# Kernel optimization log

Measured on AMD Instinct MI355X. Metric: run time of the kernel, lower is better.

## Reference

```python
import jax, jax.numpy as jnp
from jax import lax
import numpy as np

DIM = 8          # per-head dim
BN_EPS = 1e-5
ATT_EPS = 1e-15


def setup_inputs() -> dict:
    key = jax.random.key(0)
    ks = jax.random.split(key, 6)
    B, C, H, W = 2, 512, 128, 128
    total_dim = 512                      # heads(64) * dim(8)
    c3 = 3 * total_dim                   # 1536
    x = jax.random.normal(ks[0], (B, C, H, W), dtype=jnp.float32)
    w_qkv = jax.random.normal(ks[1], (c3, C), dtype=jnp.float32) * 0.02
    w_dw = jax.random.normal(ks[2], (c3, 1, 5, 5), dtype=jnp.float32) * 0.05
    w_pw = jax.random.normal(ks[3], (c3, 8, 1, 1), dtype=jnp.float32) * 0.1
    w_proj = jax.random.normal(ks[4], (512, 2 * total_dim), dtype=jnp.float32) * 0.02
    bn_gamma = jnp.ones((512,), jnp.float32)
    bn_beta = jnp.zeros((512,), jnp.float32)
    bn_mean = jnp.zeros((512,), jnp.float32)
    bn_var = jnp.ones((512,), jnp.float32)
    return {"x": x, "w_qkv": w_qkv, "w_dw": w_dw, "w_pw": w_pw, "w_proj": w_proj,
            "bn_gamma": bn_gamma, "bn_beta": bn_beta, "bn_mean": bn_mean, "bn_var": bn_var}


def reference(x, w_qkv, w_dw, w_pw, w_proj, bn_gamma, bn_beta, bn_mean, bn_var):
    B, C, H, W = x.shape
    dn = ('NCHW', 'OIHW', 'NCHW')
    # qkv: 1x1 conv, no bias/norm/act
    qkv = jnp.einsum('bchw,oc->bohw', x, w_qkv)  # (B, 1536, H, W)
    # multi-scale aggregation: 5x5 depthwise + 1x1 grouped (groups = 3*heads = 192)
    y = lax.conv_general_dilated(qkv, w_dw, (1, 1), [(2, 2), (2, 2)],
                                 feature_group_count=w_dw.shape[0], dimension_numbers=dn)
    y = lax.conv_general_dilated(y, w_pw, (1, 1), [(0, 0), (0, 0)],
                                 feature_group_count=w_pw.shape[0] // w_pw.shape[1],
                                 dimension_numbers=dn)
    mqkv = jnp.concatenate([qkv, y], axis=1)  # (B, 3072, H, W)
    N = H * W
    mqkv = mqkv.reshape(B, -1, 3 * DIM, N)    # (B, 128 heads, 24, N)
    q = jax.nn.relu(mqkv[:, :, :DIM])          # (B, h, d, N)
    k = jax.nn.relu(mqkv[:, :, DIM:2 * DIM])   # (B, h, d, N)
    v = mqkv[:, :, 2 * DIM:]                   # (B, h, d, N)
    v = jnp.pad(v, ((0, 0), (0, 0), (0, 1), (0, 0)), constant_values=1.0)  # (B,h,d+1,N)
    vk = jnp.einsum('bhdn,bhen->bhde', v, k)   # v @ k^T : (B,h,d+1,d)
    out = jnp.einsum('bhde,bhen->bhdn', vk, q)  # (B,h,d+1,N)
    out = out[:, :, :-1] / (out[:, :, -1:] + ATT_EPS)  # (B,h,d,N)
    out = out.reshape(B, -1, H, W)             # (B, 1024, H, W)
    # proj: 1x1 conv + bn2d (inference-mode affine), no act
    out = jnp.einsum('bchw,oc->bohw', out, w_proj)
    inv = bn_gamma / jnp.sqrt(bn_var + BN_EPS)
    out = out * inv[None, :, None, None] + (bn_beta - bn_mean * inv)[None, :, None, None]
    return out
```

## Files before the change

### kernel.cpp

```cpp
#include <hip/hip_runtime.h>

typedef __bf16 bf16_t;
typedef __bf16 bf16x8 __attribute__((ext_vector_type(8)));
typedef __bf16 bf16x4 __attribute__((ext_vector_type(4)));
typedef float  f32x4  __attribute__((ext_vector_type(4)));
typedef _Float16 h16;
typedef _Float16 h16x2 __attribute__((ext_vector_type(2)));
typedef _Float16 h16x4 __attribute__((ext_vector_type(4)));
typedef _Float16 h16x8 __attribute__((ext_vector_type(8)));

#define DEVINL __device__ __forceinline__

static constexpr size_t N_PIX = 16384;

static constexpr size_t OFF_QB  = 0;
static constexpr size_t SZ_QB   = (size_t)512 * N_PIX * 2;
static constexpr size_t OFF_QR  = OFF_QB + SZ_QB;
static constexpr size_t SZ_QR   = SZ_QB;
static constexpr size_t OFF_KV  = OFF_QR + SZ_QR;
static constexpr size_t SZ_KV   = (size_t)1024 * N_PIX * 2;
static constexpr size_t OFF_Y   = OFF_KV + SZ_KV;
static constexpr size_t SZ_Y    = (size_t)1536 * N_PIX * 2;
static constexpr size_t OFF_ATT = OFF_Y + SZ_Y;
static constexpr size_t SZ_ATT  = (size_t)N_PIX * 1024 * 2;
static constexpr size_t OFF_XTH = OFF_ATT;
static constexpr size_t OFF_XTL = OFF_ATT + (size_t)N_PIX * 512 * 2;
static constexpr size_t OFF_WQA = OFF_ATT + SZ_ATT;
static constexpr size_t SZ_WQA  = (size_t)512 * 1536 * 2;
static constexpr size_t OFF_WKV = OFF_WQA + SZ_WQA;
static constexpr size_t SZ_WKV  = (size_t)1024 * 512 * 2;
static constexpr size_t OFF_WP  = OFF_WKV + SZ_WKV;
static constexpr size_t SZ_WP   = (size_t)512 * 1024 * 2;
static constexpr size_t OFF_VK  = OFF_WP + SZ_WP;
static constexpr size_t SZ_VK   = (size_t)128 * 72 * 4;
static constexpr size_t OFF_VKP = OFF_VK + SZ_VK;
static constexpr size_t SZ_VKP  = (size_t)128 * 8 * 72 * 4;
static constexpr size_t OFF_BNA = OFF_VKP + SZ_VKP;
static constexpr size_t OFF_ZP  = OFF_BNA + 2048;
static constexpr size_t OFF_W2  = OFF_ZP + 64;
static constexpr size_t SZ_W2   = (size_t)512 * 1024 * 2;
static constexpr size_t WS_NEEDED = OFF_W2 + SZ_W2;

DEVINL void gload16(const void* g, void* l) {
  __builtin_amdgcn_global_load_lds((const __attribute__((address_space(1))) void*)g,
                                   (__attribute__((address_space(3))) void*)l, 16, 0, 0);
}

__global__ __launch_bounds__(256)
void xpose_kernel(const float* __restrict__ x, bf16_t* __restrict__ xTh, bf16_t* __restrict__ xTl) {
  __shared__ float t[32][33];
  const int n0 = blockIdx.x * 32, c0 = blockIdx.y * 32;
  const int tx = threadIdx.x & 31, ty = threadIdx.x >> 5;
#pragma unroll
  for (int r = 0; r < 4; ++r)
    t[ty + r * 8][tx] = x[(size_t)(c0 + ty + r * 8) * N_PIX + n0 + tx];
  __syncthreads();
  const int nl = threadIdx.x >> 3, sub = threadIdx.x & 7;
  const int c8 = (sub & 3) * 8, plane = sub >> 2;
  bf16x8 o;
#pragma unroll
  for (int k = 0; k < 8; ++k) {
    const float v = t[c8 + k][nl];
    if (plane == 0) {
      o[k] = (bf16_t)v;
    } else {
      const bf16_t hi = (bf16_t)v;
      o[k] = (bf16_t)(v - (float)hi);
    }
  }
  bf16_t* dst = plane ? xTl : xTh;
  *(bf16x8*)&dst[(size_t)(n0 + nl) * 512 + c0 + c8] = o;
}

static constexpr int PREP_W1 = 512 * 1536;
static constexpr int PREP_W2 = 1024 * 512;
static constexpr int PREP_W3 = 512 * 1024;
static constexpr int PREP_TOT = PREP_W1 + PREP_W2 + PREP_W3 + 512 + 16;
__global__ __launch_bounds__(256)
void prep_kernel(const float* __restrict__ wq, const float* __restrict__ wp,
                 const float* __restrict__ gam, const float* __restrict__ bet,
                 const float* __restrict__ mu, const float* __restrict__ va,
                 bf16_t* __restrict__ wqA, bf16_t* __restrict__ wkv, bf16_t* __restrict__ wpb,
                 float* __restrict__ bna, float* __restrict__ zp) {
  const int i = blockIdx.x * 256 + threadIdx.x;
  if (i < PREP_W1) {
    const int r = i / 1536, c = i - r * 1536;
    const int o = (r >> 3) * 24 + (r & 7);
    bf16_t out;
    if (c < 512) {
      out = (bf16_t)wq[o * 512 + c];
    } else if (c < 1024) {
      const float v = wq[o * 512 + c - 512];
      const bf16_t hi = (bf16_t)v;
      out = (bf16_t)(v - (float)hi);
    } else {
      out = (bf16_t)wq[o * 512 + c - 1024];
    }
    wqA[i] = out;
  } else if (i < PREP_W1 + PREP_W2) {
    const int j = i - PREP_W1;
    const int r = j >> 9, c = j & 511;
    const int h = (r & 511) >> 3;
    const int jj = (r < 512 ? 8 : 16) + (r & 7);
    wkv[j] = (bf16_t)wq[(h * 24 + jj) * 512 + c];
  } else if (i < PREP_W1 + PREP_W2 + PREP_W3) {
    const int j = i - PREP_W1 - PREP_W2;
    const int m = j >> 10;
    const float inv = gam[m] / sqrtf(va[m] + 1e-5f);
    wpb[j] = (bf16_t)(wp[j] * inv);
  } else if (i < PREP_W1 + PREP_W2 + PREP_W3 + 512) {
    const int k = i - PREP_W1 - PREP_W2 - PREP_W3;
    const float inv = gam[k] / sqrtf(va[k] + 1e-5f);
    bna[k] = bet[k] - mu[k] * inv;
  } else if (i < PREP_TOT) {
    zp[i - (PREP_W1 + PREP_W2 + PREP_W3 + 512)] = 0.f;
  }
}

__global__ __launch_bounds__(256, 4)
void gemm_qkv_kernel(const bf16_t* __restrict__ wqA, const bf16_t* __restrict__ wkv,
                     const bf16_t* __restrict__ xTh, const bf16_t* __restrict__ xTl,
                     h16* __restrict__ Qb, h16* __restrict__ Qr, h16* __restrict__ KV) {
  __shared__ __align__(16) bf16_t As[128 * 64];
  __shared__ __align__(16) bf16_t Bs[128 * 64];
  const int tid = threadIdx.x, wid = tid >> 6, lane = tid & 63;
  const int fr = lane & 15, fg = lane >> 4;
  const int wm = (wid >> 1) * 64, wn = (wid & 1) * 64;
  const int by = blockIdx.y;
  const bool isQ = by < 4;
  const int m0 = (isQ ? by : by - 4) * 128;
  const int n0 = blockIdx.x * 128;
  const int KA = isQ ? 1536 : 512;
  const bf16_t* Aptr = isQ ? wqA + (size_t)m0 * 1536 : wkv + (size_t)m0 * 512;
  const int srow = tid >> 3;
  const int soff = (((tid & 7) ^ (srow & 7)) * 8);

  f32x4 acc[4][4] = {};

  for (int kk = 0; kk < KA; kk += 64) {
    const bf16_t* Bpl;
    int bcol;
    if (isQ) {
      Bpl  = (kk < 1024) ? xTh : xTl;
      bcol = (kk < 1024) ? (kk & 511) : (kk - 1024);
    } else {
      Bpl = xTh; bcol = kk;
    }
    __syncthreads();
#pragma unroll
    for (int r = 0; r < 4; ++r) {
      gload16(Aptr + (size_t)(srow + 32 * r) * KA + kk + soff, As + (wid * 8 + 32 * r) * 64);
      gload16(Bpl + (size_t)(n0 + srow + 32 * r) * 512 + bcol + soff, Bs + (wid * 8 + 32 * r) * 64);
    }
    __syncthreads();
#pragma unroll
    for (int ks = 0; ks < 2; ++ks) {
      bf16x8 af[4], bfr[4];
#pragma unroll
      for (int i = 0; i < 4; ++i)
        af[i]  = *(const bf16x8*)&As[(wm + i * 16 + fr) * 64 + (((ks * 4 + fg) ^ (fr & 7)) * 8)];
#pragma unroll
      for (int j = 0; j < 4; ++j)
        bfr[j] = *(const bf16x8*)&Bs[(wn + j * 16 + fr) * 64 + (((ks * 4 + fg) ^ (fr & 7)) * 8)];
#pragma unroll
      for (int i = 0; i < 4; ++i)
#pragma unroll
        for (int j = 0; j < 4; ++j)
          acc[i][j] = __builtin_amdgcn_mfma_f32_16x16x32_bf16(af[i], bfr[j], acc[i][j], 0, 0, 0);
    }
  }

#pragma unroll
  for (int i = 0; i < 4; ++i)
#pragma unroll
    for (int r = 0; r < 4; ++r) {
      const int m = m0 + wm + i * 16 + fg * 4 + r;
#pragma unroll
      for (int j = 0; j < 4; ++j) {
        const int n = n0 + wn + j * 16 + fr;
        const float v = acc[i][j][r];
        if (isQ) {
          Qb[(size_t)m * N_PIX + n] = (h16)v;
          Qr[(size_t)m * N_PIX + n] = (h16)fmaxf(0.f, v);
        } else {
          KV[(size_t)m * N_PIX + n] = (h16)v;
        }
      }
    }
}

__global__ __launch_bounds__(256, 4)
void gemm_proj_kernel(const bf16_t* __restrict__ A, const bf16_t* __restrict__ B,
                      float* __restrict__ Cout, const float* __restrict__ bna) {
  __shared__ __align__(16) bf16_t As[128 * 64];
  __shared__ __align__(16) bf16_t Bs[128 * 64];
  const int tid = threadIdx.x, wid = tid >> 6, lane = tid & 63;
  const int fr = lane & 15, fg = lane >> 4;
  const int wm = (wid >> 1) * 64, wn = (wid & 1) * 64;
  const int m0 = blockIdx.y * 128, n0 = blockIdx.x * 128;
  const int srow = tid >> 3;
  const int soff = (((tid & 7) ^ (srow & 7)) * 8);
  const bf16_t* Ab = A + (size_t)m0 * 1024;
  const bf16_t* Bb = B + (size_t)n0 * 1024;

  f32x4 acc[4][4] = {};

  for (int kk = 0; kk < 1024; kk += 64) {
    __syncthreads();
#pragma unroll
    for (int r = 0; r < 4; ++r) {
      gload16(Ab + (size_t)(srow + 32 * r) * 1024 + kk + soff, As + (wid * 8 + 32 * r) * 64);
      gload16(Bb + (size_t)(srow + 32 * r) * 1024 + kk + soff, Bs + (wid * 8 + 32 * r) * 64);
    }
    __syncthreads();
#pragma unroll
    for (int ks = 0; ks < 2; ++ks) {
      bf16x8 af[4], bfr[4];
#pragma unroll
      for (int i = 0; i < 4; ++i)
        af[i]  = *(const bf16x8*)&As[(wm + i * 16 + fr) * 64 + (((ks * 4 + fg) ^ (fr & 7)) * 8)];
#pragma unroll
      for (int j = 0; j < 4; ++j)
        bfr[j] = *(const bf16x8*)&Bs[(wn + j * 16 + fr) * 64 + (((ks * 4 + fg) ^ (fr & 7)) * 8)];
#pragma unroll
      for (int i = 0; i < 4; ++i)
#pragma unroll
        for (int j = 0; j < 4; ++j)
          acc[i][j] = __builtin_amdgcn_mfma_f32_16x16x32_bf16(af[i], bfr[j], acc[i][j], 0, 0, 0);
    }
  }

#pragma unroll
  for (int i = 0; i < 4; ++i)
#pragma unroll
    for (int r = 0; r < 4; ++r) {
      const int m = m0 + wm + i * 16 + fg * 4 + r;
      const float sh = bna[m];
#pragma unroll
      for (int j = 0; j < 4; ++j)
        Cout[(size_t)m * N_PIX + n0 + wn + j * 16 + fr] = acc[i][j][r] + sh;
    }
}

__global__ __launch_bounds__(256)
void dwpw_kernel(const h16* __restrict__ Qb, const h16* __restrict__ KV,
                 const float* __restrict__ wdw, const float* __restrict__ wpw,
                 const h16* __restrict__ zp, h16* __restrict__ y) {
  const int g = blockIdx.y, t = blockIdx.x;
  const int typ = g % 3, head = g / 3;
  const int ty0 = (t >> 1) * 16, tx0 = (t & 1) * 64;
  const int tid = threadIdx.x, wid = tid >> 6, lane = tid & 63;
  __shared__ __align__(16) h16 sin_[8][20][80];
  __shared__ h16x2 swd2[8][25];
  __shared__ h16x2 swp2[8][8];
  if (tid < 200) {
    const h16 w = (h16)wdw[(g * 8 + tid / 25) * 25 + tid % 25];
    h16x2 w2; w2[0] = w; w2[1] = w;
    swd2[tid / 25][tid % 25] = w2;
  }
  if (tid < 64) {
    const h16 w = (h16)wpw[(g * 8 + (tid >> 3)) * 8 + (tid & 7)];
    h16x2 w2; w2[0] = w; w2[1] = w;
    swp2[tid >> 3][tid & 7] = w2;
  }
  const h16* plane = (typ == 0) ? (Qb + (size_t)head * 8 * N_PIX)
                                : (KV + (size_t)((typ == 2 ? 512 : 0) + head * 8) * N_PIX);
  h16* sflat = &sin_[0][0][0];
  for (int base = wid * 64; base < 1600; base += 256) {
    const int id  = base + lane;
    const int ch  = id / 200;
    const int rem = id - ch * 200;
    const int row = rem / 10;
    const int c6  = rem - row * 10;
    const int gy  = ty0 + row - 2;
    const int gx  = tx0 + c6 * 8 - 8;
    const bool ok = ((unsigned)gy < 128u) && ((unsigned)gx < 128u);
    const h16* src = ok ? (plane + (size_t)ch * N_PIX + gy * 128 + gx) : zp;
    gload16(src, sflat + (size_t)base * 8);
  }
  __syncthreads();

  const int px4 = (tid & 15) * 4, py = tid >> 4;
  h16x2 dwa[8][2];
#pragma unroll
  for (int ch = 0; ch < 8; ++ch) {
    h16x2 A0 = 0, A1 = 0;
#pragma unroll
    for (int di = 0; di < 5; ++di) {
      const uint2 w0 = *(const uint2*)&sin_[ch][py + di][px4 + 4];
      const uint2 w1 = *(const uint2*)&sin_[ch][py + di][px4 + 8];
      const uint2 w2v = *(const uint2*)&sin_[ch][py + di][px4 + 12];
      const unsigned u1 = w0.y, u2 = w1.x, u3 = w1.y, u4 = w2v.x;
      const h16x2 P2 = __builtin_bit_cast(h16x2, u1);
      const h16x2 P3 = __builtin_bit_cast(h16x2, (u2 << 16) | (u1 >> 16));
      const h16x2 P4 = __builtin_bit_cast(h16x2, u2);
      const h16x2 P5 = __builtin_bit_cast(h16x2, (u3 << 16) | (u2 >> 16));
      const h16x2 P6 = __builtin_bit_cast(h16x2, u3);
      const h16x2 P7 = __builtin_bit_cast(h16x2, (u4 << 16) | (u3 >> 16));
      const h16x2 P8 = __builtin_bit_cast(h16x2, u4);
      h16x2 wd;
      wd = swd2[ch][di * 5 + 0]; A0 += wd * P2; A1 += wd * P4;
      wd = swd2[ch][di * 5 + 1]; A0 += wd * P3; A1 += wd * P5;
      wd = swd2[ch][di * 5 + 2]; A0 += wd * P4; A1 += wd * P6;
      wd = swd2[ch][di * 5 + 3]; A0 += wd * P5; A1 += wd * P7;
      wd = swd2[ch][di * 5 + 4]; A0 += wd * P6; A1 += wd * P8;
    }
    dwa[ch][0] = A0; dwa[ch][1] = A1;
  }
#pragma unroll
  for (int oc = 0; oc < 8; ++oc) {
    h16x2 o0 = 0, o1 = 0;
#pragma unroll
    for (int ic = 0; ic < 8; ++ic) {
      const h16x2 w = swp2[oc][ic];
      o0 += w * dwa[ic][0];
      o1 += w * dwa[ic][1];
    }
    h16x4 ov; ov[0] = o0[0]; ov[1] = o0[1]; ov[2] = o1[0]; ov[3] = o1[1];
    *(h16x4*)&y[(size_t)(8 * g + oc) * N_PIX + (ty0 + py) * 128 + tx0 + px4] = ov;
  }
}

__global__ __launch_bounds__(256)
void vk_partial_kernel(const h16* __restrict__ KV, const h16* __restrict__ yb,
                       float* __restrict__ part) {
  const int h = blockIdx.y, s = blockIdx.x;
  const h16 *kb, *vb;
  if (h < 64) {
    kb = KV + (size_t)(h * 8) * N_PIX;
    vb = KV + (size_t)(512 + h * 8) * N_PIX;
  } else {
    kb = yb + (size_t)(24 * (h - 64) + 8) * N_PIX;
    vb = yb + (size_t)(24 * (h - 64) + 16) * N_PIX;
  }
  float a[8][8] = {};
  float ak[8] = {};
  const int p0 = s * 2048 + (int)threadIdx.x * 8;
  float kq[8][8], vq[8][8];
#pragma unroll
  for (int e = 0; e < 8; ++e) {
    h16x8 kk = *(const h16x8*)&kb[(size_t)e * N_PIX + p0];
#pragma unroll
    for (int u = 0; u < 8; ++u) kq[e][u] = fmaxf(0.f, (float)kk[u]);
  }
#pragma unroll
  for (int d = 0; d < 8; ++d) {
    h16x8 vv = *(const h16x8*)&vb[(size_t)d * N_PIX + p0];
#pragma unroll
    for (int u = 0; u < 8; ++u) vq[d][u] = (float)vv[u];
  }
#pragma unroll
  for (int d = 0; d < 8; ++d)
#pragma unroll
    for (int e = 0; e < 8; ++e)
#pragma unroll
      for (int u = 0; u < 8; ++u) a[d][e] += vq[d][u] * kq[e][u];
#pragma unroll
  for (int e = 0; e < 8; ++e)
#pragma unroll
    for (int u = 0; u < 8; ++u) ak[e] += kq[e][u];

  __shared__ float red[4][72];
  const int lane = threadIdx.x & 63, wid = threadIdx.x >> 6;
#pragma unroll
  for (int i = 0; i < 72; ++i) {
    float v = (i < 64) ? a[i >> 3][i & 7] : ak[i - 64];
    v += __shfl_xor(v, 32); v += __shfl_xor(v, 16); v += __shfl_xor(v, 8);
    v += __shfl_xor(v, 4);  v += __shfl_xor(v, 2);  v += __shfl_xor(v, 1);
    if (lane == 0) red[wid][i] = v;
  }
  __syncthreads();
  if (threadIdx.x < 72) {
    const float sum_ = red[0][threadIdx.x] + red[1][threadIdx.x] + red[2][threadIdx.x] + red[3][threadIdx.x];
    part[((size_t)h * 8 + s) * 72 + threadIdx.x] = sum_;
  }
}

__global__ __launch_bounds__(128)
void vk_reduce_kernel(const float* __restrict__ part, float* __restrict__ vk) {
  const int h = blockIdx.x;
  const int i = threadIdx.x;
  if (i < 72) {
    float s = 0.f;
#pragma unroll
    for (int t = 0; t < 8; ++t) s += part[((size_t)h * 8 + t) * 72 + i];
    vk[(size_t)h * 72 + i] = s;
  }
}

__global__ __launch_bounds__(256)
void w2_kernel(const bf16_t* __restrict__ wpb, const float* __restrict__ vkm,
               bf16_t* __restrict__ W2) {
  const int idx = blockIdx.x * 256 + threadIdx.x;
  const int m = idx >> 10, c = idx & 1023;
  const int h = c >> 3, e = c & 7;
  float s = 0.f;
#pragma unroll
  for (int d = 0; d < 8; ++d)
    s += (float)wpb[(size_t)m * 1024 + h * 8 + d] * vkm[h * 72 + d * 8 + e];
  W2[idx] = (bf16_t)s;
}

__global__ __launch_bounds__(256)
void qn_kernel(const h16* __restrict__ Qr, const h16* __restrict__ yb,
               const float* __restrict__ vk, bf16_t* __restrict__ qnT) {
  const int n0 = blockIdx.x * 32;
  const int tid = threadIdx.x;
  const int px = tid & 31, hl = tid >> 5;
  __shared__ __align__(16) bf16_t att_s[32 * 512];
  __shared__ float ak_s[64];
  for (int grp = 0; grp < 2; ++grp) {
    for (int hg = 0; hg < 8; ++hg) {
      __syncthreads();
      if (tid < 64)
        ak_s[tid] = vk[((size_t)grp * 64 + hg * 8 + (tid >> 3)) * 72 + 64 + (tid & 7)];
      __syncthreads();
      const int hh = hg * 8 + hl;
      float q[8];
      if (grp == 0) {
        const h16* plane = Qr + (size_t)(hh * 8) * N_PIX + n0 + px;
#pragma unroll
        for (int e = 0; e < 8; ++e) q[e] = (float)plane[(size_t)e * N_PIX];
      } else {
        const h16* plane = yb + (size_t)(24 * hh) * N_PIX + n0 + px;
#pragma unroll
        for (int e = 0; e < 8; ++e) q[e] = fmaxf(0.f, (float)plane[(size_t)e * N_PIX]);
      }
      float den = 1e-15f;
#pragma unroll
      for (int e = 0; e < 8; ++e) den += ak_s[hl * 8 + e] * q[e];
      const float rden = 1.0f / den;
      bf16x8 r8;
#pragma unroll
      for (int e = 0; e < 8; ++e) r8[e] = (bf16_t)(q[e] * rden);
      const int chunk = hg * 8 + hl;
      *(bf16x8*)&att_s[px * 512 + ((chunk ^ (px & 7)) << 3)] = r8;
    }
    __syncthreads();
    bf16_t* dst = qnT + (size_t)n0 * 1024 + grp * 512;
    for (int i = tid; i < 2048; i += 256) {
      const int r = i >> 6, cc = i & 63;
      bf16x8 v = *(const bf16x8*)&att_s[r * 512 + (((cc ^ (r & 7))) << 3)];
      *(bf16x8*)&dst[(size_t)r * 1024 + cc * 8] = v;
    }
  }
}

extern "C" void kernel_launch(void* const* d_in, const int* in_sizes, int n_in,
                              void* d_out, int out_size, void* d_ws, size_t ws_size,
                              hipStream_t stream) {
  if (ws_size < WS_NEEDED) return;
  const float* x      = (const float*)d_in[0];
  const float* w_qkv  = (const float*)d_in[1];
  const float* w_dw   = (const float*)d_in[2];
  const float* w_pw   = (const float*)d_in[3];
  const float* w_proj = (const float*)d_in[4];
  const float* gam    = (const float*)d_in[5];
  const float* bet    = (const float*)d_in[6];
  const float* mu     = (const float*)d_in[7];
  const float* va     = (const float*)d_in[8];

  char* w = (char*)d_ws;
  h16*    Qb   = (h16*)(w + OFF_QB);
  h16*    Qr   = (h16*)(w + OFF_QR);
  h16*    KV   = (h16*)(w + OFF_KV);
  h16*    yb   = (h16*)(w + OFF_Y);
  bf16_t* xTh  = (bf16_t*)(w + OFF_XTH);
  bf16_t* xTl  = (bf16_t*)(w + OFF_XTL);
  bf16_t* qnT  = (bf16_t*)(w + OFF_ATT);
  bf16_t* wqA  = (bf16_t*)(w + OFF_WQA);
  bf16_t* wkv  = (bf16_t*)(w + OFF_WKV);
  bf16_t* wpb  = (bf16_t*)(w + OFF_WP);
  bf16_t* W2   = (bf16_t*)(w + OFF_W2);
  float*  vk   = (float*)(w + OFF_VK);
  float*  part = (float*)(w + OFF_VKP);
  float*  bna  = (float*)(w + OFF_BNA);
  float*  zp   = (float*)(w + OFF_ZP);

  dim3 blk(256);
  prep_kernel<<<dim3((PREP_TOT + 255) / 256), blk, 0, stream>>>(
      w_qkv, w_proj, gam, bet, mu, va, wqA, wkv, wpb, bna, zp);

  for (int b = 0; b < 2; ++b) {
    const float* xb = x + (size_t)b * 512 * N_PIX;
    float* outb = (float*)d_out + (size_t)b * 512 * N_PIX;
    xpose_kernel<<<dim3(512, 16), blk, 0, stream>>>(xb, xTh, xTl);
    gemm_qkv_kernel<<<dim3(128, 12), blk, 0, stream>>>(wqA, wkv, xTh, xTl, Qb, Qr, KV);
    dwpw_kernel<<<dim3(16, 192), blk, 0, stream>>>(Qb, KV, w_dw, w_pw, (const h16*)zp, yb);
    vk_partial_kernel<<<dim3(8, 128), blk, 0, stream>>>(KV, yb, part);
    vk_reduce_kernel<<<dim3(128), dim3(128), 0, stream>>>(part, vk);
    w2_kernel<<<dim3(512 * 1024 / 256), blk, 0, stream>>>(wpb, vk, W2);
    qn_kernel<<<dim3(512), blk, 0, stream>>>(Qr, yb, vk, qnT);
    gemm_proj_kernel<<<dim3(128, 4), blk, 0, stream>>>(W2, qnT, outb, bna);
  }
}
```

Baseline: 350.2 us.

## Use single-pass fp16 QKV GEMM with selective fp32 recompute of near-zero queries

Replaces the split-precision bf16 Q GEMM (hi/lo planes, K=1536) with a single fp16 pass over K=512 for all of Q, K and V. This removes the extra two-thirds of the Q projection work. To recover accuracy it adds a detect kernel that lists (head, pixel) entries whose relu'd query is small, and a fix kernel that recomputes those entries in fp32 from the original weights and the hi+lo fp16 split of x. The GEMM epilogue now stages the tile through shared memory for vectorized 16-byte stores. The correction list is capped, so accuracy depends on how many entries fall under the threshold, and the two extra kernel launches and the atomics add overhead.

```diff
diff --git a/kernel.cpp b/kernel.cpp
--- a/kernel.cpp
+++ b/kernel.cpp
@@ -2,7 +2,6 @@
 
 typedef __bf16 bf16_t;
 typedef __bf16 bf16x8 __attribute__((ext_vector_type(8)));
-typedef __bf16 bf16x4 __attribute__((ext_vector_type(4)));
 typedef float  f32x4  __attribute__((ext_vector_type(4)));
 typedef _Float16 h16;
 typedef _Float16 h16x2 __attribute__((ext_vector_type(2)));
@@ -12,6 +11,8 @@
 #define DEVINL __device__ __forceinline__
 
 static constexpr size_t N_PIX = 16384;
+static constexpr int    FIX_CAP = 32768;
+static constexpr float  FIX_TAU = 2.5e-3f;
 
 static constexpr size_t OFF_QB  = 0;
 static constexpr size_t SZ_QB   = (size_t)512 * N_PIX * 2;
@@ -23,13 +24,11 @@
 static constexpr size_t SZ_Y    = (size_t)1536 * N_PIX * 2;
 static constexpr size_t OFF_ATT = OFF_Y + SZ_Y;
 static constexpr size_t SZ_ATT  = (size_t)N_PIX * 1024 * 2;
-static constexpr size_t OFF_XTH = OFF_ATT;
+static constexpr size_t OFF_XT  = OFF_ATT;
 static constexpr size_t OFF_XTL = OFF_ATT + (size_t)N_PIX * 512 * 2;
-static constexpr size_t OFF_WQA = OFF_ATT + SZ_ATT;
-static constexpr size_t SZ_WQA  = (size_t)512 * 1536 * 2;
-static constexpr size_t OFF_WKV = OFF_WQA + SZ_WQA;
-static constexpr size_t SZ_WKV  = (size_t)1024 * 512 * 2;
-static constexpr size_t OFF_WP  = OFF_WKV + SZ_WKV;
+static constexpr size_t OFF_WALL= OFF_ATT + SZ_ATT;
+static constexpr size_t SZ_WALL = (size_t)1536 * 512 * 2;
+static constexpr size_t OFF_WP  = OFF_WALL + SZ_WALL;
 static constexpr size_t SZ_WP   = (size_t)512 * 1024 * 2;
 static constexpr size_t OFF_VK  = OFF_WP + SZ_WP;
 static constexpr size_t SZ_VK   = (size_t)128 * 72 * 4;
@@ -39,7 +38,9 @@
 static constexpr size_t OFF_ZP  = OFF_BNA + 2048;
 static constexpr size_t OFF_W2  = OFF_ZP + 64;
 static constexpr size_t SZ_W2   = (size_t)512 * 1024 * 2;
-static constexpr size_t WS_NEEDED = OFF_W2 + SZ_W2;
+static constexpr size_t OFF_CNT = OFF_W2 + SZ_W2;
+static constexpr size_t OFF_LST = OFF_CNT + 64;
+static constexpr size_t WS_NEEDED = OFF_LST + (size_t)2 * FIX_CAP * 4;
 
 DEVINL void gload16(const void* g, void* l) {
   __builtin_amdgcn_global_load_lds((const __attribute__((address_space(1))) void*)g,
@@ -47,7 +48,7 @@
 }
 
 __global__ __launch_bounds__(256)
-void xpose_kernel(const float* __restrict__ x, bf16_t* __restrict__ xTh, bf16_t* __restrict__ xTl) {
+void xpose_kernel(const float* __restrict__ x, h16* __restrict__ xT, h16* __restrict__ xTl) {
   __shared__ float t[32][33];
   const int n0 = blockIdx.x * 32, c0 = blockIdx.y * 32;
   const int tx = threadIdx.x & 31, ty = threadIdx.x >> 5;
@@ -57,136 +58,179 @@
   __syncthreads();
   const int nl = threadIdx.x >> 3, sub = threadIdx.x & 7;
   const int c8 = (sub & 3) * 8, plane = sub >> 2;
-  bf16x8 o;
+  h16x8 o;
 #pragma unroll
   for (int k = 0; k < 8; ++k) {
     const float v = t[c8 + k][nl];
     if (plane == 0) {
-      o[k] = (bf16_t)v;
+      o[k] = (h16)v;
     } else {
-      const bf16_t hi = (bf16_t)v;
-      o[k] = (bf16_t)(v - (float)hi);
-    }
-  }
-  bf16_t* dst = plane ? xTl : xTh;
-  *(bf16x8*)&dst[(size_t)(n0 + nl) * 512 + c0 + c8] = o;
-}
-
-static constexpr int PREP_W1 = 512 * 1536;
-static constexpr int PREP_W2 = 1024 * 512;
-static constexpr int PREP_W3 = 512 * 1024;
-static constexpr int PREP_TOT = PREP_W1 + PREP_W2 + PREP_W3 + 512 + 16;
+      const h16 hi = (h16)v;
+      o[k] = (h16)(v - (float)hi);
+    }
+  }
+  h16* dst = plane ? xTl : xT;
+  *(h16x8*)&dst[(size_t)(n0 + nl) * 512 + c0 + c8] = o;
+}
+
+static constexpr int PREP_P1 = 1536 * 512;
+static constexpr int PREP_P2 = 512 * 1024;
+static constexpr int PREP_TOT = PREP_P1 + PREP_P2 + 512 + 16 + 2;
 __global__ __launch_bounds__(256)
 void prep_kernel(const float* __restrict__ wq, const float* __restrict__ wp,
                  const float* __restrict__ gam, const float* __restrict__ bet,
                  const float* __restrict__ mu, const float* __restrict__ va,
-                 bf16_t* __restrict__ wqA, bf16_t* __restrict__ wkv, bf16_t* __restrict__ wpb,
-                 float* __restrict__ bna, float* __restrict__ zp) {
+                 h16* __restrict__ wall, bf16_t* __restrict__ wpb,
+                 float* __restrict__ bna, float* __restrict__ zp, int* __restrict__ cnt) {
   const int i = blockIdx.x * 256 + threadIdx.x;
-  if (i < PREP_W1) {
-    const int r = i / 1536, c = i - r * 1536;
-    const int o = (r >> 3) * 24 + (r & 7);
-    bf16_t out;
-    if (c < 512) {
-      out = (bf16_t)wq[o * 512 + c];
-    } else if (c < 1024) {
-      const float v = wq[o * 512 + c - 512];
-      const bf16_t hi = (bf16_t)v;
-      out = (bf16_t)(v - (float)hi);
-    } else {
-      out = (bf16_t)wq[o * 512 + c - 1024];
-    }
-    wqA[i] = out;
-  } else if (i < PREP_W1 + PREP_W2) {
-    const int j = i - PREP_W1;
-    const int r = j >> 9, c = j & 511;
-    const int h = (r & 511) >> 3;
-    const int jj = (r < 512 ? 8 : 16) + (r & 7);
-    wkv[j] = (bf16_t)wq[(h * 24 + jj) * 512 + c];
-  } else if (i < PREP_W1 + PREP_W2 + PREP_W3) {
-    const int j = i - PREP_W1 - PREP_W2;
+  if (i < PREP_P1) {
+    const int r = i >> 9, c = i & 511;
+    int o;
+    if (r < 512)       o = (r >> 3) * 24 + (r & 7);
+    else if (r < 1024) o = ((r - 512) >> 3) * 24 + 8 + (r & 7);
+    else               o = ((r - 1024) >> 3) * 24 + 16 + (r & 7);
+    wall[i] = (h16)wq[(size_t)o * 512 + c];
+  } else if (i < PREP_P1 + PREP_P2) {
+    const int j = i - PREP_P1;
     const int m = j >> 10;
     const float inv = gam[m] / sqrtf(va[m] + 1e-5f);
     wpb[j] = (bf16_t)(wp[j] * inv);
-  } else if (i < PREP_W1 + PREP_W2 + PREP_W3 + 512) {
-    const int k = i - PREP_W1 - PREP_W2 - PREP_W3;
+  } else if (i < PREP_P1 + PREP_P2 + 512) {
+    const int k = i - PREP_P1 - PREP_P2;
     const float inv = gam[k] / sqrtf(va[k] + 1e-5f);
     bna[k] = bet[k] - mu[k] * inv;
+  } else if (i < PREP_P1 + PREP_P2 + 512 + 16) {
+    zp[i - (PREP_P1 + PREP_P2 + 512)] = 0.f;
   } else if (i < PREP_TOT) {
-    zp[i - (PREP_W1 + PREP_W2 + PREP_W3 + 512)] = 0.f;
+    cnt[i - (PREP_P1 + PREP_P2 + 512 + 16)] = 0;
   }
 }
 
 __global__ __launch_bounds__(256, 4)
-void gemm_qkv_kernel(const bf16_t* __restrict__ wqA, const bf16_t* __restrict__ wkv,
-                     const bf16_t* __restrict__ xTh, const bf16_t* __restrict__ xTl,
+void gemm_qkv_kernel(const h16* __restrict__ wall, const h16* __restrict__ xT,
                      h16* __restrict__ Qb, h16* __restrict__ Qr, h16* __restrict__ KV) {
-  __shared__ __align__(16) bf16_t As[128 * 64];
-  __shared__ __align__(16) bf16_t Bs[128 * 64];
+  __shared__ __align__(16) h16 smem[128 * 128];
+  h16* As = smem;
+  h16* Bs = smem + 8192;
   const int tid = threadIdx.x, wid = tid >> 6, lane = tid & 63;
   const int fr = lane & 15, fg = lane >> 4;
   const int wm = (wid >> 1) * 64, wn = (wid & 1) * 64;
   const int by = blockIdx.y;
-  const bool isQ = by < 4;
-  const int m0 = (isQ ? by : by - 4) * 128;
   const int n0 = blockIdx.x * 128;
-  const int KA = isQ ? 1536 : 512;
-  const bf16_t* Aptr = isQ ? wqA + (size_t)m0 * 1536 : wkv + (size_t)m0 * 512;
+  const h16* Aptr = wall + (size_t)by * 128 * 512;
   const int srow = tid >> 3;
   const int soff = (((tid & 7) ^ (srow & 7)) * 8);
 
   f32x4 acc[4][4] = {};
 
-  for (int kk = 0; kk < KA; kk += 64) {
-    const bf16_t* Bpl;
-    int bcol;
+  for (int kk = 0; kk < 512; kk += 64) {
+    __syncthreads();
+#pragma unroll
+    for (int r = 0; r < 4; ++r) {
+      gload16(Aptr + (size_t)(srow + 32 * r) * 512 + kk + soff, As + (wid * 8 + 32 * r) * 64);
+      gload16(xT + (size_t)(n0 + srow + 32 * r) * 512 + kk + soff, Bs + (wid * 8 + 32 * r) * 64);
+    }
+    __syncthreads();
+#pragma unroll
+    for (int ks = 0; ks < 2; ++ks) {
+      h16x8 af[4], bfr[4];
+#pragma unroll
+      for (int i = 0; i < 4; ++i)
+        af[i]  = *(const h16x8*)&As[(wm + i * 16 + fr) * 64 + (((ks * 4 + fg) ^ (fr & 7)) * 8)];
+#pragma unroll
+      for (int j = 0; j < 4; ++j)
+        bfr[j] = *(const h16x8*)&Bs[(wn + j * 16 + fr) * 64 + (((ks * 4 + fg) ^ (fr & 7)) * 8)];
+#pragma unroll
+      for (int i = 0; i < 4; ++i)
+#pragma unroll
+        for (int j = 0; j < 4; ++j)
+          acc[i][j] = __builtin_amdgcn_mfma_f32_16x16x32_f16(af[i], bfr[j], acc[i][j], 0, 0, 0);
+    }
+  }
+
+  __syncthreads();
+#pragma unroll
+  for (int i = 0; i < 4; ++i)
+#pragma unroll
+    for (int r = 0; r < 4; ++r) {
+      const int ml = wm + i * 16 + fg * 4 + r;
+#pragma unroll
+      for (int j = 0; j < 4; ++j) {
+        const int nl = wn + j * 16 + fr;
+        smem[ml * 128 + (nl ^ ((ml & 7) << 3))] = (h16)acc[i][j][r];
+      }
+    }
+  __syncthreads();
+
+  const int row = tid >> 1, cgrp = (tid & 1) * 64;
+  const bool isQ = by < 4;
+#pragma unroll
+  for (int k = 0; k < 8; ++k) {
+    const int col = cgrp + k * 8;
+    h16x8 v = *(const h16x8*)&smem[row * 128 + (col ^ ((row & 7) << 3))];
     if (isQ) {
-      Bpl  = (kk < 1024) ? xTh : xTl;
-      bcol = (kk < 1024) ? (kk & 511) : (kk - 1024);
+      const size_t o = (size_t)(by * 128 + row) * N_PIX + n0 + col;
+      *(h16x8*)&Qb[o] = v;
+      h16x8 rv;
+#pragma unroll
+      for (int u = 0; u < 8; ++u) rv[u] = (v[u] > (h16)0.f) ? v[u] : (h16)0.f;
+      *(h16x8*)&Qr[o] = rv;
     } else {
-      Bpl = xTh; bcol = kk;
-    }
-    __syncthreads();
-#pragma unroll
-    for (int r = 0; r < 4; ++r) {
-      gload16(Aptr + (size_t)(srow + 32 * r) * KA + kk + soff, As + (wid * 8 + 32 * r) * 64);
-      gload16(Bpl + (size_t)(n0 + srow + 32 * r) * 512 + bcol + soff, Bs + (wid * 8 + 32 * r) * 64);
-    }
-    __syncthreads();
-#pragma unroll
-    for (int ks = 0; ks < 2; ++ks) {
-      bf16x8 af[4], bfr[4];
-#pragma unroll
-      for (int i = 0; i < 4; ++i)
-        af[i]  = *(const bf16x8*)&As[(wm + i * 16 + fr) * 64 + (((ks * 4 + fg) ^ (fr & 7)) * 8)];
-#pragma unroll
-      for (int j = 0; j < 4; ++j)
-        bfr[j] = *(const bf16x8*)&Bs[(wn + j * 16 + fr) * 64 + (((ks * 4 + fg) ^ (fr & 7)) * 8)];
-#pragma unroll
-      for (int i = 0; i < 4; ++i)
-#pragma unroll
-        for (int j = 0; j < 4; ++j)
-          acc[i][j] = __builtin_amdgcn_mfma_f32_16x16x32_bf16(af[i], bfr[j], acc[i][j], 0, 0, 0);
-    }
-  }
-
-#pragma unroll
-  for (int i = 0; i < 4; ++i)
-#pragma unroll
-    for (int r = 0; r < 4; ++r) {
-      const int m = m0 + wm + i * 16 + fg * 4 + r;
-#pragma unroll
-      for (int j = 0; j < 4; ++j) {
-        const int n = n0 + wn + j * 16 + fr;
-        const float v = acc[i][j][r];
-        if (isQ) {
-          Qb[(size_t)m * N_PIX + n] = (h16)v;
-          Qr[(size_t)m * N_PIX + n] = (h16)fmaxf(0.f, v);
-        } else {
-          KV[(size_t)m * N_PIX + n] = (h16)v;
-        }
-      }
-    }
+      *(h16x8*)&KV[(size_t)((by - 4) * 128 + row) * N_PIX + n0 + col] = v;
+    }
+  }
+}
+
+__global__ __launch_bounds__(256)
+void detect_kernel(const h16* __restrict__ Qr, int* __restrict__ cnt, int* __restrict__ list) {
+  const int h = blockIdx.y;
+  const int n = blockIdx.x * 256 + threadIdx.x;
+  float m = 0.f;
+#pragma unroll
+  for (int e = 0; e < 8; ++e)
+    m = fmaxf(m, (float)Qr[(size_t)(h * 8 + e) * N_PIX + n]);
+  if (m < FIX_TAU) {
+    const int idx = atomicAdd(cnt, 1);
+    if (idx < FIX_CAP) list[idx] = (h << 14) | n;
+  }
+}
+
+__global__ __launch_bounds__(256)
+void fix_kernel(const float* __restrict__ wq, const h16* __restrict__ xT,
+                const h16* __restrict__ xTl, const int* __restrict__ cnt,
+                const int* __restrict__ list, h16* __restrict__ Qr) {
+  __shared__ float red[4][8];
+  const int tid = threadIdx.x, lane = tid & 63, wid = tid >> 6;
+  int total = *cnt;
+  if (total > FIX_CAP) total = FIX_CAP;
+  for (int gi = blockIdx.x; gi < total; gi += gridDim.x) {
+    const int ent = list[gi];
+    const int h = ent >> 14, n = ent & 16383;
+    const int c0 = tid * 2;
+    const h16x2 xh = *(const h16x2*)&xT[(size_t)n * 512 + c0];
+    const h16x2 xl = *(const h16x2*)&xTl[(size_t)n * 512 + c0];
+    const float x0 = (float)xh[0] + (float)xl[0];
+    const float x1 = (float)xh[1] + (float)xl[1];
+    float acc[8];
+#pragma unroll
+    for (int e = 0; e < 8; ++e) {
+      const float2 wv = *(const float2*)&wq[(size_t)(h * 24 + e) * 512 + c0];
+      acc[e] = wv.x * x0 + wv.y * x1;
+    }
+#pragma unroll
+    for (int e = 0; e < 8; ++e) {
+      float v = acc[e];
+      v += __shfl_xor(v, 32); v += __shfl_xor(v, 16); v += __shfl_xor(v, 8);
+      v += __shfl_xor(v, 4);  v += __shfl_xor(v, 2);  v += __shfl_xor(v, 1);
+      if (lane == 0) red[wid][e] = v;
+    }
+    __syncthreads();
+    if (tid < 8) {
+      const float q = red[0][tid] + red[1][tid] + red[2][tid] + red[3][tid];
+      Qr[(size_t)(h * 8 + tid) * N_PIX + n] = (h16)fmaxf(0.f, q);
+    }
+    __syncthreads();
+  }
 }
 
 __global__ __launch_bounds__(256, 4)
@@ -465,27 +509,30 @@
   h16*    Qr   = (h16*)(w + OFF_QR);
   h16*    KV   = (h16*)(w + OFF_KV);
   h16*    yb   = (h16*)(w + OFF_Y);
-  bf16_t* xTh  = (bf16_t*)(w + OFF_XTH);
-  bf16_t* xTl  = (bf16_t*)(w + OFF_XTL);
+  h16*    xT   = (h16*)(w + OFF_XT);
+  h16*    xTl  = (h16*)(w + OFF_XTL);
   bf16_t* qnT  = (bf16_t*)(w + OFF_ATT);
-  bf16_t* wqA  = (bf16_t*)(w + OFF_WQA);
-  bf16_t* wkv  = (bf16_t*)(w + OFF_WKV);
+  h16*    wall = (h16*)(w + OFF_WALL);
   bf16_t* wpb  = (bf16_t*)(w + OFF_WP);
   bf16_t* W2   = (bf16_t*)(w + OFF_W2);
   float*  vk   = (float*)(w + OFF_VK);
   float*  part = (float*)(w + OFF_VKP);
   float*  bna  = (float*)(w + OFF_BNA);
   float*  zp   = (float*)(w + OFF_ZP);
+  int*    cnt  = (int*)(w + OFF_CNT);
+  int*    list = (int*)(w + OFF_LST);
 
   dim3 blk(256);
   prep_kernel<<<dim3((PREP_TOT + 255) / 256), blk, 0, stream>>>(
-      w_qkv, w_proj, gam, bet, mu, va, wqA, wkv, wpb, bna, zp);
+      w_qkv, w_proj, gam, bet, mu, va, wall, wpb, bna, zp, cnt);
 
   for (int b = 0; b < 2; ++b) {
     const float* xb = x + (size_t)b * 512 * N_PIX;
     float* outb = (float*)d_out + (size_t)b * 512 * N_PIX;
-    xpose_kernel<<<dim3(512, 16), blk, 0, stream>>>(xb, xTh, xTl);
-    gemm_qkv_kernel<<<dim3(128, 12), blk, 0, stream>>>(wqA, wkv, xTh, xTl, Qb, Qr, KV);
+    xpose_kernel<<<dim3(512, 16), blk, 0, stream>>>(xb, xT, xTl);
+    gemm_qkv_kernel<<<dim3(128, 12), blk, 0, stream>>>(wall, xT, Qb, Qr, KV);
+    detect_kernel<<<dim3(64, 64), blk, 0, stream>>>(Qr, cnt + b, list + (size_t)b * FIX_CAP);
+    fix_kernel<<<dim3(2048), blk, 0, stream>>>(w_qkv, xT, xTl, cnt + b, list + (size_t)b * FIX_CAP, Qr);
     dwpw_kernel<<<dim3(16, 192), blk, 0, stream>>>(Qb, KV, w_dw, w_pw, (const h16*)zp, yb);
     vk_partial_kernel<<<dim3(8, 128), blk, 0, stream>>>(KV, yb, part);
     vk_reduce_kernel<<<dim3(128), dim3(128), 0, stream>>>(part, vk);
```

New measurement: 464.0 us. +32.5%, slower.
